# Kernel tuning notes

Hardware: AMD Instinct MI355X
Metric: run time of the kernel (lower is better)

Reference implementation:

```python
import jax, jax.numpy as jnp
import numpy as np

B, S, D = 1, 4096, 768
H = 12
HD = D // H  # 64


def setup_inputs() -> dict:
    key = jax.random.key(0)
    ks = jax.random.split(key, 6)
    sc = 1.0 / np.sqrt(D)
    return {
        "x": jax.random.normal(ks[0], (B, S, D), dtype=jnp.float32),
        "wq": jax.random.normal(ks[1], (D, D), dtype=jnp.float32) * sc,
        "wk": jax.random.normal(ks[2], (D, D), dtype=jnp.float32) * sc,
        "wv": jax.random.normal(ks[3], (D, D), dtype=jnp.float32) * sc,
        "wo": jax.random.normal(ks[4], (D, D), dtype=jnp.float32) * sc,
        "bo": jax.random.normal(ks[5], (D,), dtype=jnp.float32) * 0.02,
    }


def reference(x, wq, wk, wv, wo, bo):
    b, n, _ = x.shape
    # projections (torch Linear: x @ W.T; here weights stored as (d_in, d_out))
    q = (x @ wq).reshape(b, n, H, HD).transpose(0, 2, 1, 3)  # b h n d
    k = (x @ wk).reshape(b, n, H, HD).transpose(0, 2, 1, 3)
    v = (x @ wv).reshape(b, n, H, HD).transpose(0, 2, 1, 3)
    scores = jnp.einsum("bhqd,bhkd->bhqk", q, k)
    causal = jnp.tril(jnp.ones((n, n), dtype=bool))  # True = keep
    scores = jnp.where(causal, scores, -jnp.inf)
    weights = jax.nn.softmax(scores / np.sqrt(HD), axis=-1)
    ctx = jnp.einsum("bhqk,bhkd->bhqd", weights, v)
    ctx = ctx.transpose(0, 2, 1, 3).reshape(b, n, D)
    return ctx @ wo + bo
```

## Files before the change

kernel.cpp:

```cpp
#include <hip/hip_runtime.h>


typedef short bf16x8 __attribute__((ext_vector_type(8)));
typedef float f32x4 __attribute__((ext_vector_type(4)));
typedef unsigned short u16;

static constexpr int S_LEN = 4096;
static constexpr int DIM   = 768;
static constexpr int NH    = 12;
static constexpr float QSCALE = 0.125f * 1.44269504088896340736f;

__device__ inline u16 f2bf(float f) {
  union { float f; unsigned int u; } v; v.f = f;
  unsigned int r = v.u + 0x7FFFu + ((v.u >> 16) & 1u);
  return (u16)(r >> 16);
}

__device__ inline void gload_lds16(const u16* g, u16* s) {
  __builtin_amdgcn_global_load_lds(
      (const __attribute__((address_space(1))) unsigned int*)g,
      (__attribute__((address_space(3))) unsigned int*)s, 16, 0, 0);
}

__global__ __launch_bounds__(256)
void prep_kernel(const float* __restrict__ x, const float* __restrict__ w0,
                 const float* __restrict__ w1, const float* __restrict__ w2,
                 const float* __restrict__ w3, u16* __restrict__ xb,
                 u16* __restrict__ t0, u16* __restrict__ t1,
                 u16* __restrict__ t2, u16* __restrict__ t3) {
  if (blockIdx.z == 4) {
    const size_t n = (size_t)S_LEN * DIM;
    const int id = blockIdx.y * 12 + blockIdx.x;
    const size_t stride = (size_t)144 * 256 * 8;
    for (size_t i = ((size_t)id * 256 + threadIdx.x) * 8; i < n; i += stride) {
      const float4 a = *(const float4*)(x + i);
      const float4 b = *(const float4*)(x + i + 4);
      bf16x8 o;
      o[0] = (short)f2bf(a.x); o[1] = (short)f2bf(a.y);
      o[2] = (short)f2bf(a.z); o[3] = (short)f2bf(a.w);
      o[4] = (short)f2bf(b.x); o[5] = (short)f2bf(b.y);
      o[6] = (short)f2bf(b.z); o[7] = (short)f2bf(b.w);
      *(bf16x8*)(xb + i) = o;
    }
    return;
  }
  __shared__ float T[64][65];
  const float* src; u16* dst;
  switch (blockIdx.z) {
    case 0: src = w0; dst = t0; break;
    case 1: src = w1; dst = t1; break;
    case 2: src = w2; dst = t2; break;
    default: src = w3; dst = t3; break;
  }
  const int k0 = blockIdx.y * 64, n0 = blockIdx.x * 64;
  const int r = threadIdx.x >> 2, c0 = (threadIdx.x & 3) * 16;
#pragma unroll
  for (int i = 0; i < 4; ++i) {
    const float4 v = *(const float4*)(src + (size_t)(k0 + r) * DIM + n0 + c0 + i * 4);
    T[r][c0 + i * 4 + 0] = v.x;
    T[r][c0 + i * 4 + 1] = v.y;
    T[r][c0 + i * 4 + 2] = v.z;
    T[r][c0 + i * 4 + 3] = v.w;
  }
  __syncthreads();
  bf16x8 o0, o1;
#pragma unroll
  for (int i = 0; i < 8; ++i) {
    o0[i] = (short)f2bf(T[c0 + i][r]);
    o1[i] = (short)f2bf(T[c0 + 8 + i][r]);
  }
  *(bf16x8*)(dst + (size_t)(n0 + r) * DIM + k0 + c0) = o0;
  *(bf16x8*)(dst + (size_t)(n0 + r) * DIM + k0 + c0 + 8) = o1;
}

template <int MODE>
__global__ __launch_bounds__(256)
void mfma_gemm_kernel(const u16* __restrict__ A, const u16* __restrict__ Bq,
                      const u16* __restrict__ Bk, const u16* __restrict__ Bv,
                      const float* __restrict__ bias, u16* __restrict__ Qb,
                      u16* __restrict__ Kb, u16* __restrict__ VT,
                      float* __restrict__ Out) {
  constexpr int MT = (MODE == 0) ? 4 : 2;
  constexpr int BM = MT * 32;
  __shared__ __align__(16) u16 Al[BM * 64];
  __shared__ __align__(16) u16 Bl[96 * 64];

  const int tid  = threadIdx.x;
  const int wv   = tid >> 6;
  const int lane = tid & 63;
  const int quad = lane >> 4;
  const int l16  = lane & 15;
  const int wr = wv >> 1, wc = wv & 1;
  const int m0 = blockIdx.y * BM;
  const int n0 = blockIdx.x * 96;

  int wi = 0, nb = n0;
  const u16* BT = Bq;
  if (MODE == 0) {
    wi = n0 / DIM;
    nb = n0 - wi * DIM;
    BT = (wi == 0) ? Bq : (wi == 1) ? Bk : Bv;
  }

  const int sr8 = lane >> 3;
  const int sc  = ((lane & 7) ^ sr8) * 8;
  const int key = l16 & 7;

  const bool swp = (MODE == 1) || (wi < 2);

  f32x4 acc[MT][3] = {};

  for (int k0 = 0; k0 < DIM; k0 += 64) {
    __syncthreads();
#pragma unroll
    for (int j = 0; j < MT; ++j)
      gload_lds16(A + (size_t)(m0 + wv * (BM / 4) + j * 8 + sr8) * DIM + k0 + sc,
                  &Al[(wv * (BM / 4) + j * 8) * 64]);
#pragma unroll
    for (int j = 0; j < 3; ++j)
      gload_lds16(BT + (size_t)(nb + wv * 24 + j * 8 + sr8) * DIM + k0 + sc,
                  &Bl[(wv * 24 + j * 8) * 64]);
    __syncthreads();

#pragma unroll
    for (int kh = 0; kh < 2; ++kh) {
      const int cb = kh * 4;
      bf16x8 af[MT], bfr[3];
#pragma unroll
      for (int mt = 0; mt < MT; ++mt) {
        const int row = wr * (BM / 2) + mt * 16 + l16;
        af[mt] = *(const bf16x8*)&Al[row * 64 + ((cb + quad) ^ key) * 8];
      }
#pragma unroll
      for (int nt = 0; nt < 3; ++nt) {
        const int row = wc * 48 + nt * 16 + l16;
        bfr[nt] = *(const bf16x8*)&Bl[row * 64 + ((cb + quad) ^ key) * 8];
      }
      if (swp) {
#pragma unroll
        for (int mt = 0; mt < MT; ++mt)
#pragma unroll
          for (int nt = 0; nt < 3; ++nt)
            acc[mt][nt] = __builtin_amdgcn_mfma_f32_16x16x32_bf16(
                bfr[nt], af[mt], acc[mt][nt], 0, 0, 0);
      } else {
#pragma unroll
        for (int mt = 0; mt < MT; ++mt)
#pragma unroll
          for (int nt = 0; nt < 3; ++nt)
            acc[mt][nt] = __builtin_amdgcn_mfma_f32_16x16x32_bf16(
                af[mt], bfr[nt], acc[mt][nt], 0, 0, 0);
      }
    }
  }

  if (MODE == 0 && wi >= 2) {
#pragma unroll
    for (int mt = 0; mt < MT; ++mt) {
#pragma unroll
      for (int nt = 0; nt < 3; ++nt) {
        const int row  = m0 + wr * (BM / 2) + mt * 16 + quad * 4;
        const int ncol = nb + wc * 48 + nt * 16 + l16;
        u16 pk[4];
#pragma unroll
        for (int r = 0; r < 4; ++r) pk[r] = f2bf(acc[mt][nt][r]);
        unsigned long long v;
        __builtin_memcpy(&v, pk, 8);
        *(unsigned long long*)(VT + (size_t)ncol * S_LEN + row) = v;
      }
    }
  } else if (MODE == 0) {
    u16* dst = (wi == 0) ? Qb : Kb;
    const float sc_out = (wi == 0) ? QSCALE : 1.0f;
#pragma unroll
    for (int mt = 0; mt < MT; ++mt) {
#pragma unroll
      for (int nt = 0; nt < 3; ++nt) {
        const int row = m0 + wr * (BM / 2) + mt * 16 + l16;
        const int ncb = nb + wc * 48 + nt * 16 + quad * 4;
        u16 pk[4];
#pragma unroll
        for (int r = 0; r < 4; ++r) pk[r] = f2bf(acc[mt][nt][r] * sc_out);
        unsigned long long v;
        __builtin_memcpy(&v, pk, 8);
        *(unsigned long long*)(dst + (size_t)row * DIM + ncb) = v;
      }
    }
  } else {
#pragma unroll
    for (int mt = 0; mt < MT; ++mt) {
#pragma unroll
      for (int nt = 0; nt < 3; ++nt) {
        const int row = m0 + wr * (BM / 2) + mt * 16 + l16;
        const int ncb = n0 + wc * 48 + nt * 16 + quad * 4;
        const float4 b4 = *(const float4*)(bias + ncb);
        float4 ov;
        ov.x = acc[mt][nt][0] + b4.x;
        ov.y = acc[mt][nt][1] + b4.y;
        ov.z = acc[mt][nt][2] + b4.z;
        ov.w = acc[mt][nt][3] + b4.w;
        *(float4*)(Out + (size_t)row * DIM + ncb) = ov;
      }
    }
  }
}

__global__ __launch_bounds__(256, 5)
void attn_mfma_kernel(const u16* __restrict__ Qb, const u16* __restrict__ Kb,
                      const u16* __restrict__ VTb, float* __restrict__ pbuf) {
  __shared__ __align__(16) u16 KVl[128 * 64 + 64 * 128];
  u16* const Kl = KVl;
  u16* const Vl = KVl + 128 * 64;

  const int tid  = threadIdx.x;
  const int w    = tid >> 6;
  const int lane = tid & 63;
  const int quad = lane >> 4;
  const int l16  = lane & 15;
  const int qw   = w >> 1;
  const int kw   = w & 1;
  const int key  = l16 & 7;

  const int id = blockIdx.x;
  const int h  = id % 12;
  const int j  = id / 12;
  const int ck = j & 3;
  const int to = j >> 2;
  const int qt = 127 - to;
  const int q0 = qt * 32;

  const int nkt = qt / 2 + 1;
  const int niter = (nkt + 1) >> 1;
  const int my_last = nkt - 1;

  const int i0 = ck * 8;
  if (i0 >= niter) return;
  const int i1 = (i0 + 8 < niter) ? (i0 + 8) : niter;

  const int sr8  = lane >> 3;
  const int scK  = ((lane & 7) ^ sr8) * 8;
  const int sr16 = lane >> 4;

  const u16* qptr = Qb + (size_t)(q0 + qw * 16 + l16) * DIM + h * 64 + quad * 8;
  const bf16x8 aq0 = *(const bf16x8*)(qptr);
  const bf16x8 aq1 = *(const bf16x8*)(qptr + 32);

  f32x4 o[4] = {};
  float l_s = 0.f;
  const int qg = q0 + qw * 16 + l16;

#pragma unroll 1
  for (int i = i0; i < i1; ++i) {
    const int k0g = i * 128;
    asm volatile("s_waitcnt lgkmcnt(0)" ::: "memory");
    __builtin_amdgcn_s_barrier();

#pragma unroll
    for (int jj = 0; jj < 4; ++jj)
      gload_lds16(Kb + (size_t)(k0g + w * 32 + jj * 8 + sr8) * DIM + h * 64 + scK,
                  &Kl[(w * 32 + jj * 8) * 64]);
#pragma unroll
    for (int jj = 0; jj < 4; ++jj) {
      const int vrow = w * 16 + jj * 4 + sr16;
      const int vcol = ((lane & 15) ^ (vrow & 7)) * 8;
      gload_lds16(VTb + (size_t)(h * 64 + vrow) * S_LEN + k0g + vcol,
                  &Vl[(w * 16 + jj * 4) * 128]);
    }
    asm volatile("s_waitcnt vmcnt(4)" ::: "memory");
    __builtin_amdgcn_s_barrier();

    const int kt_w = 2 * i + kw;
    const bool act = kt_w < nkt;
    bf16x8 pa0, pa1;
    if (act) {
      __builtin_amdgcn_s_setprio(1);
      f32x4 s[4];
#pragma unroll
      for (int t = 0; t < 4; ++t) {
        const int row = kw * 64 + t * 16 + l16;
        const bf16x8 bk0 = *(const bf16x8*)&Kl[row * 64 + (quad ^ key) * 8];
        const bf16x8 bk1 = *(const bf16x8*)&Kl[row * 64 + ((quad ^ 4) ^ key) * 8];
        s[t] = __builtin_amdgcn_mfma_f32_16x16x32_bf16(
            bk0, aq0, f32x4{0.f, 0.f, 0.f, 0.f}, 0, 0, 0);
        s[t] = __builtin_amdgcn_mfma_f32_16x16x32_bf16(bk1, aq1, s[t], 0, 0, 0);
      }

      unsigned Wt[4][2];
      if (kt_w == my_last) {
#pragma unroll
        for (int t = 0; t < 4; ++t) {
          float pr[4];
#pragma unroll
          for (int r = 0; r < 4; ++r) {
            const int kvg = k0g + kw * 64 + t * 16 + quad * 4 + r;
            float p = __builtin_amdgcn_exp2f(s[t][r]);
            if (kvg > qg) p = 0.f;
            l_s += p;
            pr[r] = p;
          }
          asm("v_cvt_pk_bf16_f32 %0, %1, %2" : "=v"(Wt[t][0]) : "v"(pr[0]), "v"(pr[1]));
          asm("v_cvt_pk_bf16_f32 %0, %1, %2" : "=v"(Wt[t][1]) : "v"(pr[2]), "v"(pr[3]));
        }
      } else {
#pragma unroll
        for (int t = 0; t < 4; ++t) {
          float pr[4];
#pragma unroll
          for (int r = 0; r < 4; ++r) {
            const float p = __builtin_amdgcn_exp2f(s[t][r]);
            l_s += p;
            pr[r] = p;
          }
          asm("v_cvt_pk_bf16_f32 %0, %1, %2" : "=v"(Wt[t][0]) : "v"(pr[0]), "v"(pr[1]));
          asm("v_cvt_pk_bf16_f32 %0, %1, %2" : "=v"(Wt[t][1]) : "v"(pr[2]), "v"(pr[3]));
        }
      }

      {
        unsigned a0 = Wt[0][0], b0 = Wt[1][0];
        unsigned a1 = Wt[0][1], b1 = Wt[1][1];
        asm("v_permlane32_swap_b32 %0, %1" : "+v"(a0), "+v"(b0));
        asm("v_permlane16_swap_b32 %0, %1" : "+v"(a0), "+v"(b0));
        asm("v_permlane32_swap_b32 %0, %1" : "+v"(a1), "+v"(b1));
        asm("v_permlane16_swap_b32 %0, %1" : "+v"(a1), "+v"(b1));
        union { unsigned u[4]; bf16x8 v; } U0;
        U0.u[0] = a0; U0.u[1] = a1; U0.u[2] = b0; U0.u[3] = b1;
        pa0 = U0.v;
        unsigned c0 = Wt[2][0], d0 = Wt[3][0];
        unsigned c1 = Wt[2][1], d1 = Wt[3][1];
        asm("v_permlane32_swap_b32 %0, %1" : "+v"(c0), "+v"(d0));
        asm("v_permlane16_swap_b32 %0, %1" : "+v"(c0), "+v"(d0));
        asm("v_permlane32_swap_b32 %0, %1" : "+v"(c1), "+v"(d1));
        asm("v_permlane16_swap_b32 %0, %1" : "+v"(c1), "+v"(d1));
        union { unsigned u[4]; bf16x8 v; } U1;
        U1.u[0] = c0; U1.u[1] = c1; U1.u[2] = d0; U1.u[3] = d1;
        pa1 = U1.v;
      }
    }

    asm volatile("s_waitcnt vmcnt(0)" ::: "memory");
    __builtin_amdgcn_s_barrier();

    if (act) {
#pragma unroll
      for (int t = 0; t < 4; ++t) {
        const int row = t * 16 + l16;
        const int cc0 = (kw * 8 + quad) ^ key;
        const int cc1 = (kw * 8 + quad + 4) ^ key;
        const bf16x8 vb0 = *(const bf16x8*)&Vl[row * 128 + cc0 * 8];
        const bf16x8 vb1 = *(const bf16x8*)&Vl[row * 128 + cc1 * 8];
        o[t] = __builtin_amdgcn_mfma_f32_16x16x32_bf16(pa0, vb0, o[t], 0, 0, 0);
        o[t] = __builtin_amdgcn_mfma_f32_16x16x32_bf16(pa1, vb1, o[t], 0, 0, 0);
      }
      __builtin_amdgcn_s_setprio(0);
    }
  }

  __syncthreads();
  float* Obuf  = (float*)KVl;
  float* lbufF = Obuf + 5120;
#pragma unroll
  for (int t = 0; t < 4; ++t)
    *(f32x4*)&Obuf[(w * 64 + lane) * 20 + t * 4] = o[t];
  lbufF[w * 64 + lane] = l_s;
  __syncthreads();
#pragma unroll
  for (int t = 0; t < 4; ++t) {
    const f32x4 po = *(const f32x4*)&Obuf[((w ^ 1) * 64 + lane) * 20 + t * 4];
    o[t] += po;
  }
  l_s += lbufF[(w ^ 1) * 64 + lane];

  if (kw == 0) {
    float L = l_s;
    L += __shfl_xor(L, 16);
    L += __shfl_xor(L, 32);
    float* pe = pbuf + ((size_t)(to * 4 + ck) * 12 + h) * 2080;
    if (quad == 0) pe[2048 + qw * 16 + l16] = L;
#pragma unroll
    for (int r = 0; r < 4; ++r) {
      const int row = qw * 16 + quad * 4 + r;
#pragma unroll
      for (int t = 0; t < 4; ++t)
        pe[row * 64 + t * 16 + l16] = o[t][r];
    }
  }
}

__global__ __launch_bounds__(256)
void attn_combine(const float* __restrict__ pbuf, u16* __restrict__ ctx) {
  const int id = blockIdx.x;
  const int h  = id % 12;
  const int to = id / 12;
  const int qt = 127 - to;
  const int niter = (qt / 2 + 2) >> 1;
  const int nch = (niter + 7) >> 3;

  const int row = threadIdx.x >> 3;
  const int dc  = (threadIdx.x & 7) * 8;

  f32x4 a0 = {}, a1 = {};
  float lsum = 0.f;
  for (int c = 0; c < nch; ++c) {
    const float* pe = pbuf + ((size_t)(to * 4 + c) * 12 + h) * 2080;
    a0 += *(const f32x4*)(pe + row * 64 + dc);
    a1 += *(const f32x4*)(pe + row * 64 + dc + 4);
    lsum += pe[2048 + row];
  }
  const float inv = 1.f / lsum;
  bf16x8 ov;
#pragma unroll
  for (int jj = 0; jj < 4; ++jj) {
    ov[jj]     = (short)f2bf(a0[jj] * inv);
    ov[jj + 4] = (short)f2bf(a1[jj] * inv);
  }
  *(bf16x8*)(ctx + (size_t)(qt * 32 + row) * DIM + h * 64 + dc) = ov;
}

extern "C" void kernel_launch(void* const* d_in, const int* in_sizes, int n_in,
                              void* d_out, int out_size, void* d_ws,
                              size_t ws_size, hipStream_t stream) {
  const float* x  = (const float*)d_in[0];
  const float* wq = (const float*)d_in[1];
  const float* wk = (const float*)d_in[2];
  const float* wv = (const float*)d_in[3];
  const float* wo = (const float*)d_in[4];
  const float* bo = (const float*)d_in[5];

  const size_t n_x = (size_t)S_LEN * DIM;
  const size_t n_w = (size_t)DIM * DIM;
  u16* xb  = (u16*)d_ws;
  u16* wtq = xb + n_x;
  u16* wtk = wtq + n_w;
  u16* wtv = wtk + n_w;
  u16* wto = wtv + n_w;
  u16* Qb  = wto + n_w;
  u16* Kb  = Qb + n_x;
  u16* VTb = Kb + n_x;
  u16* ctx = VTb + n_x;
  float* pbuf = (float*)(ctx + n_x);

  prep_kernel<<<dim3(12, 12, 5), 256, 0, stream>>>(
      x, wq, wk, wv, wo, xb, wtq, wtk, wtv, wto);

  mfma_gemm_kernel<0><<<dim3(24, 32), 256, 0, stream>>>(
      xb, wtq, wtk, wtv, nullptr, Qb, Kb, VTb, nullptr);

  attn_mfma_kernel<<<dim3(6144), 256, 0, stream>>>(Qb, Kb, VTb, pbuf);

  attn_combine<<<dim3(1536), 256, 0, stream>>>(pbuf, ctx);

  mfma_gemm_kernel<1><<<dim3(8, 64), 256, 0, stream>>>(
      ctx, wto, nullptr, nullptr, bo, nullptr, nullptr, nullptr, (float*)d_out);
}
```

Baseline: 170.6 us.

## Rebalance causal attention split-K: halve long tiles, write short tiles directly

Replaces the fixed 4-way key-chunk split (6144 blocks, many of which exit early) with a scheme where the 64 longest query tiles are split into two halves and the remaining tiles run unsplit. Unsplit blocks normalize and write bf16 context directly, and the combine kernel only merges two partials for 768 blocks. This cuts empty-block launches, partial-buffer traffic and combine work, at the risk of more load imbalance because each block now processes longer key ranges.

```diff
diff --git a/kernel.cpp b/kernel.cpp
--- a/kernel.cpp
+++ b/kernel.cpp
@@ -207,7 +207,8 @@
 
 __global__ __launch_bounds__(256, 5)
 void attn_mfma_kernel(const u16* __restrict__ Qb, const u16* __restrict__ Kb,
-                      const u16* __restrict__ VTb, float* __restrict__ pbuf) {
+                      const u16* __restrict__ VTb, u16* __restrict__ ctx,
+                      float* __restrict__ pbuf) {
   __shared__ __align__(16) u16 KVl[128 * 64 + 64 * 128];
   u16* const Kl = KVl;
   u16* const Vl = KVl + 128 * 64;
@@ -222,10 +223,21 @@
   const int key  = l16 & 7;
 
   const int id = blockIdx.x;
-  const int h  = id % 12;
-  const int j  = id / 12;
-  const int ck = j & 3;
-  const int to = j >> 2;
+  int to, ck, h;
+  bool split;
+  if (id < 1536) {
+    to = id / 24;
+    const int rest = id - to * 24;
+    ck = rest / 12;
+    h  = rest - ck * 12;
+    split = true;
+  } else {
+    const int jd = id - 1536;
+    to = 64 + jd / 12;
+    h  = jd % 12;
+    ck = 0;
+    split = false;
+  }
   const int qt = 127 - to;
   const int q0 = qt * 32;
 
@@ -233,9 +245,12 @@
   const int niter = (nkt + 1) >> 1;
   const int my_last = nkt - 1;
 
-  const int i0 = ck * 8;
-  if (i0 >= niter) return;
-  const int i1 = (i0 + 8 < niter) ? (i0 + 8) : niter;
+  int i0 = 0, i1 = niter;
+  if (split) {
+    const int half = (niter + 1) >> 1;
+    i0 = ck ? half : 0;
+    i1 = ck ? niter : half;
+  }
 
   const int sr8  = lane >> 3;
   const int scK  = ((lane & 7) ^ sr8) * 8;
@@ -372,17 +387,31 @@
   l_s += lbufF[(w ^ 1) * 64 + lane];
 
   if (kw == 0) {
-    float L = l_s;
-    L += __shfl_xor(L, 16);
-    L += __shfl_xor(L, 32);
-    float* pe = pbuf + ((size_t)(to * 4 + ck) * 12 + h) * 2080;
-    if (quad == 0) pe[2048 + qw * 16 + l16] = L;
-#pragma unroll
-    for (int r = 0; r < 4; ++r) {
-      const int row = qw * 16 + quad * 4 + r;
-#pragma unroll
-      for (int t = 0; t < 4; ++t)
-        pe[row * 64 + t * 16 + l16] = o[t][r];
+    if (!split) {
+      float L = l_s;
+      L += __shfl_xor(L, 16);
+      L += __shfl_xor(L, 32);
+#pragma unroll
+      for (int r = 0; r < 4; ++r) {
+        const float inv = 1.f / __shfl(L, quad * 4 + r);
+        const int row = q0 + qw * 16 + quad * 4 + r;
+#pragma unroll
+        for (int t = 0; t < 4; ++t)
+          ctx[(size_t)row * DIM + h * 64 + t * 16 + l16] = f2bf(o[t][r] * inv);
+      }
+    } else {
+      float L = l_s;
+      L += __shfl_xor(L, 16);
+      L += __shfl_xor(L, 32);
+      float* pe = pbuf + ((size_t)(to * 2 + ck) * 12 + h) * 2080;
+      if (quad == 0) pe[2048 + qw * 16 + l16] = L;
+#pragma unroll
+      for (int r = 0; r < 4; ++r) {
+        const int row = qw * 16 + quad * 4 + r;
+#pragma unroll
+        for (int t = 0; t < 4; ++t)
+          pe[row * 64 + t * 16 + l16] = o[t][r];
+      }
     }
   }
 }
@@ -393,20 +422,19 @@
   const int h  = id % 12;
   const int to = id / 12;
   const int qt = 127 - to;
-  const int niter = (qt / 2 + 2) >> 1;
-  const int nch = (niter + 7) >> 3;
 
   const int row = threadIdx.x >> 3;
   const int dc  = (threadIdx.x & 7) * 8;
 
-  f32x4 a0 = {}, a1 = {};
-  float lsum = 0.f;
-  for (int c = 0; c < nch; ++c) {
-    const float* pe = pbuf + ((size_t)(to * 4 + c) * 12 + h) * 2080;
-    a0 += *(const f32x4*)(pe + row * 64 + dc);
-    a1 += *(const f32x4*)(pe + row * 64 + dc + 4);
-    lsum += pe[2048 + row];
-  }
+  const float* p0 = pbuf + ((size_t)(to * 2 + 0) * 12 + h) * 2080;
+  const float* p1 = pbuf + ((size_t)(to * 2 + 1) * 12 + h) * 2080;
+
+  f32x4 a0 = *(const f32x4*)(p0 + row * 64 + dc);
+  f32x4 a1 = *(const f32x4*)(p0 + row * 64 + dc + 4);
+  a0 += *(const f32x4*)(p1 + row * 64 + dc);
+  a1 += *(const f32x4*)(p1 + row * 64 + dc + 4);
+  const float lsum = p0[2048 + row] + p1[2048 + row];
+
   const float inv = 1.f / lsum;
   bf16x8 ov;
 #pragma unroll
@@ -446,9 +474,9 @@
   mfma_gemm_kernel<0><<<dim3(24, 32), 256, 0, stream>>>(
       xb, wtq, wtk, wtv, nullptr, Qb, Kb, VTb, nullptr);
 
-  attn_mfma_kernel<<<dim3(6144), 256, 0, stream>>>(Qb, Kb, VTb, pbuf);
-
-  attn_combine<<<dim3(1536), 256, 0, stream>>>(pbuf, ctx);
+  attn_mfma_kernel<<<dim3(2304), 256, 0, stream>>>(Qb, Kb, VTb, ctx, pbuf);
+
+  attn_combine<<<dim3(768), 256, 0, stream>>>(pbuf, ctx);
 
   mfma_gemm_kernel<1><<<dim3(8, 64), 256, 0, stream>>>(
       ctx, wto, nullptr, nullptr, bo, nullptr, nullptr, nullptr, (float*)d_out);
```

Result: faster. 164.4 us (-3.7%).
